# Kernel optimization log

Hardware: AMD Instinct MI355X
Metric: run time of the kernel (lower is better)

## Reference

```python
import jax, jax.numpy as jnp
import numpy as np

H = 10                 # heads in both convs
EPS = 1e-5             # GraphNorm eps
N, E, D_NODE, D_EDGE, G = 100000, 1600000, 128, 32, 64


def _lin(key, out_d, in_d, bias=True):
    k1, k2 = jax.random.split(key)
    W = jax.random.normal(k1, (out_d, in_d), jnp.float32) / np.sqrt(in_d)
    if bias:
        b = jax.random.normal(k2, (out_d,), jnp.float32) * 0.01
        return W, b
    return W


def setup_inputs() -> dict:
    key = jax.random.key(0)
    ks = jax.random.split(key, 20)
    x = jax.random.normal(ks[0], (N, D_NODE), jnp.float32)
    edge_attr = jax.random.normal(ks[1], (E, D_EDGE), jnp.float32)
    edge_index = jax.random.randint(ks[2], (2, E), 0, N)
    batch_idx = jnp.sort(jax.random.randint(ks[3], (N,), 0, G))
    # conv1: in=128, out=5, heads=10
    q1W, q1b = _lin(ks[4], H * 5, D_NODE)
    k1W, k1b = _lin(ks[5], H * 5, D_NODE)
    v1W, v1b = _lin(ks[6], H * 5, D_NODE)
    e1W = _lin(ks[7], H * 5, D_EDGE, bias=False)
    s1W, s1b = _lin(ks[8], 5, D_NODE)        # lin_skip
    b1W = _lin(ks[9], 1, 3 * 5, bias=False)  # lin_beta
    # GraphNorm(5)
    gnW = jnp.ones((5,), jnp.float32)
    gnb = jnp.zeros((5,), jnp.float32)
    gnms = jnp.ones((5,), jnp.float32)       # mean_scale
    # conv2: in=5, out=1, heads=10
    q2W, q2b = _lin(ks[10], H * 1, 5)
    k2W, k2b = _lin(ks[11], H * 1, 5)
    v2W, v2b = _lin(ks[12], H * 1, 5)
    e2W = _lin(ks[13], H * 1, D_EDGE, bias=False)
    s2W, s2b = _lin(ks[14], 1, 5)
    b2W = _lin(ks[15], 1, 3 * 1, bias=False)
    return dict(x=x, edge_attr=edge_attr, edge_index=edge_index, batch_idx=batch_idx,
                q1W=q1W, q1b=q1b, k1W=k1W, k1b=k1b, v1W=v1W, v1b=v1b, e1W=e1W,
                s1W=s1W, s1b=s1b, b1W=b1W, gnW=gnW, gnb=gnb, gnms=gnms,
                q2W=q2W, q2b=q2b, k2W=k2W, k2b=k2b, v2W=v2W, v2b=v2b, e2W=e2W,
                s2W=s2W, s2b=s2b, b2W=b2W)


def _tconv(x, src, dst, edge_attr, qW, qb, kW, kb, vW, vb, eW, sW, sb, bW, c):
    """PyG TransformerConv: concat=False, beta=True, eval (dropout off)."""
    n = x.shape[0]
    q = (x @ qW.T + qb).reshape(n, H, c)
    k = (x @ kW.T + kb).reshape(n, H, c)
    v = (x @ vW.T + vb).reshape(n, H, c)
    e = (edge_attr @ eW.T).reshape(-1, H, c)            # [E,H,c]
    kj = k[src] + e                                      # gather + edge bias
    alpha = jnp.einsum('ehc,ehc->eh', q[dst], kj) / np.sqrt(c)
    amax = jax.lax.stop_gradient(jax.ops.segment_max(alpha, dst, num_segments=n))
    ex = jnp.exp(alpha - amax[dst])
    denom = jax.ops.segment_sum(ex, dst, num_segments=n)
    a = ex / denom[dst]                                  # segment softmax [E,H]
    out = jax.ops.segment_sum((v[src] + e) * a[:, :, None], dst, num_segments=n)
    out = out.mean(axis=1)                               # concat=False -> head mean [N,c]
    xr = x @ sW.T + sb                                   # skip
    beta = jax.nn.sigmoid(jnp.concatenate([out, xr, out - xr], -1) @ bW.T)
    return beta * xr + (1.0 - beta) * out


def _graph_norm(x, batch, w, b, ms):
    cnt = jnp.maximum(jax.ops.segment_sum(jnp.ones((x.shape[0],), x.dtype), batch,
                                          num_segments=G), 1.0)[:, None]
    mean = jax.ops.segment_sum(x, batch, num_segments=G) / cnt
    out = x - mean[batch] * ms
    var = jax.ops.segment_sum(out * out, batch, num_segments=G) / cnt
    return w * out / jnp.sqrt(var + EPS)[batch] + b


def reference(x, edge_attr, edge_index, batch_idx,
              q1W, q1b, k1W, k1b, v1W, v1b, e1W, s1W, s1b, b1W,
              gnW, gnb, gnms,
              q2W, q2b, k2W, k2b, v2W, v2b, e2W, s2W, s2b, b2W):
    src, dst = edge_index[0], edge_index[1]
    h = _tconv(x, src, dst, edge_attr, q1W, q1b, k1W, k1b, v1W, v1b, e1W,
               s1W, s1b, b1W, 5)
    h = jax.nn.relu(_graph_norm(h, batch_idx, gnW, gnb, gnms))
    out = _tconv(h, src, dst, edge_attr, q2W, q2b, k2W, k2b, v2W, v2b, e2W,
                 s2W, s2b, b2W, 1)
    return jax.nn.sigmoid(out)
```

## Files before the change

### kernel.cpp

```cpp
#include <hip/hip_runtime.h>
#include <math.h>


#define EPS 1e-5f
#define INV_SQRT5 0.44721359549995794f

__device__ __forceinline__ float f16_to_f32(unsigned short u) {
  union { unsigned short us; _Float16 h; } cv; cv.us = u;
  return (float)cv.h;
}

__device__ __forceinline__ void store40(const float (&acc)[40], int n, int g,
                                        float* __restrict__ q1, float* __restrict__ kv1,
                                        float* __restrict__ xr1) {
#pragma unroll
  for (int c = 0; c < 40; ++c) {
    int ch = g * 40 + c;
    if (ch < 50)        q1[(size_t)n * 52 + ch] = acc[c];
    else if (ch < 100)  kv1[(size_t)n * 104 + 2 * (ch - 50)] = acc[c];
    else if (ch < 150)  kv1[(size_t)n * 104 + 2 * (ch - 100) + 1] = acc[c];
    else if (ch < 155)  xr1[(size_t)n * 8 + (ch - 150)] = acc[c];
  }
}

__global__ __launch_bounds__(256, 3) void k_qkvs1(
    const float* __restrict__ x,
    const float* __restrict__ qW, const float* __restrict__ qb,
    const float* __restrict__ kW, const float* __restrict__ kb,
    const float* __restrict__ vW, const float* __restrict__ vb,
    const float* __restrict__ sW, const float* __restrict__ sb,
    float* __restrict__ q1, float* __restrict__ kv1,
    float* __restrict__ xr1, int n_nodes) {
  __shared__ __align__(16) float sWt[40 * 128];
  __shared__ __align__(16) float sX[512 * 20];
  __shared__ float sB[40];
  const int t = threadIdx.x;
  const int g = blockIdx.y;
  const int n0 = blockIdx.x * 512;

  for (int i = t; i < 1280; i += 256) {
    int c = i >> 5, q = i & 31;
    int ch = g * 40 + c;
    float4 w = make_float4(0.f, 0.f, 0.f, 0.f);
    const float* srcr = nullptr;
    if (ch < 50)        srcr = qW + ch * 128;
    else if (ch < 100)  srcr = kW + (ch - 50) * 128;
    else if (ch < 150)  srcr = vW + (ch - 100) * 128;
    else if (ch < 155)  srcr = sW + (ch - 150) * 128;
    if (srcr) w = *(const float4*)(srcr + q * 4);
    *(float4*)&sWt[c * 128 + q * 4] = w;
  }
  if (t < 40) {
    int ch = g * 40 + t;
    float b = 0.f;
    if (ch < 50) b = qb[ch];
    else if (ch < 100) b = kb[ch - 50];
    else if (ch < 150) b = vb[ch - 100];
    else if (ch < 155) b = sb[ch - 150];
    sB[t] = b;
  }
  __syncthreads();

  float accA[40], accB[40];
#pragma unroll
  for (int c = 0; c < 40; ++c) { accA[c] = sB[c]; accB[c] = sB[c]; }
  const int na = n0 + 2 * t, nb = na + 1;
  const float4* w4 = (const float4*)sWt;

  for (int kc = 0; kc < 128; kc += 16) {
    __syncthreads();
#pragma unroll
    for (int i = 0; i < 8; ++i) {
      int idx = t + 256 * i;
      int r = idx >> 2, q = idx & 3;
      int n = n0 + r;
      float4 v = make_float4(0.f, 0.f, 0.f, 0.f);
      if (n < n_nodes) v = *(const float4*)(x + (size_t)n * 128 + kc + q * 4);
      *(float4*)&sX[r * 20 + q * 4] = v;
    }
    __syncthreads();
    float4 xa[4], xb[4];
#pragma unroll
    for (int q = 0; q < 4; ++q) {
      xa[q] = *(const float4*)&sX[(2 * t) * 20 + q * 4];
      xb[q] = *(const float4*)&sX[(2 * t + 1) * 20 + q * 4];
    }
    int base = kc >> 2;
#pragma unroll
    for (int c = 0; c < 40; ++c) {
#pragma unroll
      for (int q = 0; q < 4; ++q) {
        float4 w = w4[c * 32 + base + q];
        accA[c] = fmaf(w.x, xa[q].x, accA[c]); accA[c] = fmaf(w.y, xa[q].y, accA[c]);
        accA[c] = fmaf(w.z, xa[q].z, accA[c]); accA[c] = fmaf(w.w, xa[q].w, accA[c]);
        accB[c] = fmaf(w.x, xb[q].x, accB[c]); accB[c] = fmaf(w.y, xb[q].y, accB[c]);
        accB[c] = fmaf(w.z, xb[q].z, accB[c]); accB[c] = fmaf(w.w, xb[q].w, accB[c]);
      }
    }
  }
  if (na < n_nodes) store40(accA, na, g, q1, kv1, xr1);
  if (nb < n_nodes) store40(accB, nb, g, q1, kv1, xr1);
}

__global__ __launch_bounds__(256) void k_hist(const int* __restrict__ ei, int n_edges,
                                              int* __restrict__ cnt) {
  int e = blockIdx.x * 256 + threadIdx.x;
  if (e < n_edges) atomicAdd(&cnt[ei[n_edges + e]], 1);
}

__global__ __launch_bounds__(1024) void k_scan(const int* __restrict__ cnt,
                                               int* __restrict__ rp,
                                               int* __restrict__ cursor, int n) {
  __shared__ int ls[1024];
  int tid = threadIdx.x;
  const int CH = (((n + 1023) / 1024) + 3) & ~3;
  int lo = tid * CH, hi = min(lo + CH, n);
  int s = 0;
  if (lo < n) {
    int full = (hi - lo) & ~3;
    const int4* c4 = (const int4*)(cnt + lo);
    for (int i = 0; i < full; i += 4) {
      int4 v = c4[i >> 2];
      s += v.x + v.y + v.z + v.w;
    }
    for (int i = lo + full; i < hi; ++i) s += cnt[i];
  }
  ls[tid] = s;
  __syncthreads();
  for (int off = 1; off < 1024; off <<= 1) {
    int v = (tid >= off) ? ls[tid - off] : 0;
    __syncthreads();
    ls[tid] += v;
    __syncthreads();
  }
  int run = (tid > 0) ? ls[tid - 1] : 0;
  for (int i = lo; i < hi; ++i) {
    rp[i] = run; cursor[i] = run; run += cnt[i];
  }
  if (hi == n && lo < n) rp[n] = run;
}

__global__ __launch_bounds__(256) void k_scatter(const int* __restrict__ ei, int n_edges,
                                                 int* __restrict__ cursor,
                                                 int* __restrict__ seid,
                                                 int* __restrict__ ssrc) {
  int e = blockIdx.x * 256 + threadIdx.x;
  if (e >= n_edges) return;
  int s = ei[e];
  int d = ei[n_edges + e];
  int p = atomicAdd(&cursor[d], 1);
  seid[p] = e;
  ssrc[p] = s;
}

__global__ __launch_bounds__(256) void k_evt(
    float* attr, const float* __restrict__ e1W, const float* __restrict__ e2W,
    int n_edges) {
  int e = blockIdx.x * 256 + threadIdx.x;
  if (e >= n_edges) return;
  const float4* ar = (const float4*)(attr + (size_t)e * 32);
  float4 a[8];
#pragma unroll
  for (int j = 0; j < 8; ++j) a[j] = ar[j];
  unsigned int d[30];
#pragma unroll
  for (int c2 = 0; c2 < 30; ++c2) {
    int c0 = 2 * c2, c1 = 2 * c2 + 1;
    const float* w0 = (c0 < 50) ? (e1W + c0 * 32) : (e2W + (c0 - 50) * 32);
    const float* w1 = (c1 < 50) ? (e1W + c1 * 32) : (e2W + (c1 - 50) * 32);
    float acc0 = 0.f, acc1 = 0.f;
#pragma unroll
    for (int j = 0; j < 8; ++j) {
      float4 wa = *(const float4*)(w0 + 4 * j);
      float4 wb = *(const float4*)(w1 + 4 * j);
      acc0 = fmaf(wa.x, a[j].x, acc0); acc0 = fmaf(wa.y, a[j].y, acc0);
      acc0 = fmaf(wa.z, a[j].z, acc0); acc0 = fmaf(wa.w, a[j].w, acc0);
      acc1 = fmaf(wb.x, a[j].x, acc1); acc1 = fmaf(wb.y, a[j].y, acc1);
      acc1 = fmaf(wb.z, a[j].z, acc1); acc1 = fmaf(wb.w, a[j].w, acc1);
    }
    union { _Float16 h[2]; unsigned int u; } p;
    p.h[0] = (_Float16)acc0; p.h[1] = (_Float16)acc1;
    d[c2] = p.u;
  }
  unsigned int* row = (unsigned int*)(attr + (size_t)e * 32);
#pragma unroll
  for (int k = 0; k < 7; ++k)
    *(uint4*)(row + 4 * k) = make_uint4(d[4 * k], d[4 * k + 1], d[4 * k + 2], d[4 * k + 3]);
  *(uint2*)(row + 28) = make_uint2(d[28], d[29]);
}

__global__ __launch_bounds__(256) void k_conv1(
    const int* __restrict__ rp, const int* __restrict__ seid,
    const int* __restrict__ ssrc, const float* __restrict__ attr,
    const float* __restrict__ q1, const float* __restrict__ kv1,
    const float* __restrict__ xr1,
    const float* __restrict__ bW, float* __restrict__ h1, int n_nodes) {
  const int lane = threadIdx.x & 63;
  const int wid = (blockIdx.x * 256 + threadIdx.x) >> 6;
  const int nw = gridDim.x * 4;
  const int wr = (lane < 50) ? lane : 0;
  const int g0 = (wr / 5) * 5;
  const int cp = lane % 5;
  const unsigned short* evr = (const unsigned short*)attr;

  for (int n = wid; n < n_nodes; n += nw) {
    const int p0 = rp[n], deg = rp[n + 1] - p0;
    const float qc = q1[(size_t)n * 52 + wr];
    int eL = 0, sL = 0;
    if (lane < deg) { eL = seid[p0 + lane]; sL = ssrc[p0 + lane]; }
    float accN = 0.f, accD = 0.f;
    for (int i = 0; i < deg; ++i) {
      int e, s;
      if (i < 64) { e = __shfl(eL, i); s = __shfl(sL, i); }
      else        { e = seid[p0 + i]; s = ssrc[p0 + i]; }
      float ev = f16_to_f32(evr[(size_t)e * 64 + wr]);
      float2 kv = *(const float2*)(kv1 + (size_t)s * 104 + 2 * wr);
      float t = qc * (kv.x + ev);
      float al = __shfl(t, g0) + __shfl(t, g0 + 1) + __shfl(t, g0 + 2)
               + __shfl(t, g0 + 3) + __shfl(t, g0 + 4);
      float ex = __expf(al * INV_SQRT5);
      accD += ex;
      accN = fmaf(kv.y + ev, ex, accN);
    }
    float r = (accD > 0.f) ? accN / accD : 0.f;
    if (lane >= 50) r = 0.f;
    float o = 0.f;
#pragma unroll
    for (int h = 0; h < 10; ++h) o += __shfl(r, cp + 5 * h);
    o *= 0.1f;
    float xr = xr1[(size_t)n * 8 + cp];
    float tb = bW[cp] * o + bW[5 + cp] * xr + bW[10 + cp] * (o - xr);
    float sb = 0.f;
#pragma unroll
    for (int j = 0; j < 5; ++j) sb += __shfl(tb, j);
    float beta = 1.f / (1.f + __expf(-sb));
    if (lane < 5) h1[(size_t)n * 8 + lane] = beta * xr + (1.f - beta) * o;
  }
}

__global__ __launch_bounds__(256) void k_stats(
    const float* __restrict__ h1, const int* __restrict__ batch,
    float* __restrict__ gsum, float* __restrict__ gsq,
    float* __restrict__ gcnt, int n_nodes) {
  int n = blockIdx.x * 256 + threadIdx.x;
  bool act = n < n_nodes;
  int g = act ? batch[n] : 0;
  float v[5], s2[5], one = act ? 1.f : 0.f;
#pragma unroll
  for (int c = 0; c < 5; ++c) {
    v[c] = act ? h1[(size_t)n * 8 + c] : 0.f;
    s2[c] = v[c] * v[c];
  }
  int g0 = __shfl(g, 0);
  bool uni = __all((!act) || (g == g0));
  if (uni) {
#pragma unroll
    for (int off = 32; off; off >>= 1) {
#pragma unroll
      for (int c = 0; c < 5; ++c) {
        v[c] += __shfl_down(v[c], off);
        s2[c] += __shfl_down(s2[c], off);
      }
      one += __shfl_down(one, off);
    }
    if ((threadIdx.x & 63) == 0) {
#pragma unroll
      for (int c = 0; c < 5; ++c) {
        atomicAdd(&gsum[g0 * 8 + c], v[c]);
        atomicAdd(&gsq[g0 * 8 + c], s2[c]);
      }
      atomicAdd(&gcnt[g0], one);
    }
  } else if (act) {
#pragma unroll
    for (int c = 0; c < 5; ++c) {
      atomicAdd(&gsum[g * 8 + c], v[c]);
      atomicAdd(&gsq[g * 8 + c], s2[c]);
    }
    atomicAdd(&gcnt[g], 1.f);
  }
}

__global__ __launch_bounds__(256) void k_apply(
    const float* __restrict__ h1, const int* __restrict__ batch,
    const float* __restrict__ gsum, const float* __restrict__ gsq,
    const float* __restrict__ gcnt,
    const float* __restrict__ gnw, const float* __restrict__ gnb,
    const float* __restrict__ gnms,
    const float* __restrict__ q2W, const float* __restrict__ q2b,
    const float* __restrict__ k2W, const float* __restrict__ k2b,
    const float* __restrict__ v2W, const float* __restrict__ v2b,
    const float* __restrict__ s2W, const float* __restrict__ s2b,
    float* __restrict__ q2, float* __restrict__ kv2,
    float* __restrict__ xr2, int n_nodes) {
  int n = blockIdx.x * 256 + threadIdx.x;
  if (n >= n_nodes) return;
  int g = batch[n];
  float rc = 1.f / fmaxf(gcnt[g], 1.f);
  float r[5];
#pragma unroll
  for (int c = 0; c < 5; ++c) {
    float ms = gnms[c];
    float mean = gsum[g * 8 + c] * rc;
    float var = gsq[g * 8 + c] * rc - mean * mean * ms * (2.f - ms);
    var = fmaxf(var, 0.f);
    float o = h1[(size_t)n * 8 + c] - mean * ms;
    float y = gnw[c] * o * rsqrtf(var + EPS) + gnb[c];
    r[c] = fmaxf(y, 0.f);
  }
#pragma unroll
  for (int h = 0; h < 10; ++h) {
    float aq = q2b[h], ak = k2b[h], av = v2b[h];
#pragma unroll
    for (int i = 0; i < 5; ++i) {
      aq = fmaf(r[i], q2W[h * 5 + i], aq);
      ak = fmaf(r[i], k2W[h * 5 + i], ak);
      av = fmaf(r[i], v2W[h * 5 + i], av);
    }
    q2[(size_t)n * 12 + h] = aq;
    kv2[(size_t)n * 24 + 2 * h]     = ak;
    kv2[(size_t)n * 24 + 2 * h + 1] = av;
  }
  float s = s2b[0];
#pragma unroll
  for (int i = 0; i < 5; ++i) s = fmaf(r[i], s2W[i], s);
  xr2[n] = s;
}

__global__ __launch_bounds__(256) void k_conv2(
    const int* __restrict__ rp, const int* __restrict__ seid,
    const int* __restrict__ ssrc, const float* __restrict__ attr,
    const float* __restrict__ q2, const float* __restrict__ kv2,
    const float* __restrict__ xr2,
    const float* __restrict__ bW, float* __restrict__ out, int n_nodes) {
  const int lane = threadIdx.x & 63;
  const int wid = (blockIdx.x * 256 + threadIdx.x) >> 6;
  const int nw = gridDim.x * 4;
  const int slot = lane / 10, h = lane - slot * 10;
  const bool active = slot < 6;
  const unsigned short* evr = (const unsigned short*)attr;

  for (int n = wid; n < n_nodes; n += nw) {
    int p0 = rp[n], deg = rp[n + 1] - p0;
    float qh = q2[(size_t)n * 12 + h];
    int eL = 0, sL = 0;
    if (lane < deg) { eL = seid[p0 + lane]; sL = ssrc[p0 + lane]; }
    float accN = 0.f, accD = 0.f;
    int nit = (deg + 5) / 6;
    for (int t = 0; t < nit; ++t) {
      int i = t * 6 + slot;
      bool val = active && (i < deg);
      int e = 0, s = 0;
      if (i < 64) { e = __shfl(eL, i); s = __shfl(sL, i); }
      else if (val) { e = seid[p0 + i]; s = ssrc[p0 + i]; }
      float evv = 0.f; float2 kv = make_float2(0.f, 0.f);
      if (val) {
        evv = f16_to_f32(evr[(size_t)e * 64 + 50 + h]);
        kv = *(const float2*)(kv2 + (size_t)s * 24 + 2 * h);
      }
      float exv = val ? __expf(qh * (kv.x + evv)) : 0.f;
      accD += exv;
      accN = fmaf(kv.y + evv, exv, accN);
    }
    float D = 0.f, Nn = 0.f;
#pragma unroll
    for (int i2 = 0; i2 < 6; ++i2) {
      D  += __shfl(accD, h + 10 * i2);
      Nn += __shfl(accN, h + 10 * i2);
    }
    float r = (D > 0.f) ? Nn / D : 0.f;
    float o = 0.f;
#pragma unroll
    for (int j = 0; j < 10; ++j) o += __shfl(r, j);
    o *= 0.1f;
    float xr = xr2[n];
    float sbv = bW[0] * o + bW[1] * xr + bW[2] * (o - xr);
    float beta = 1.f / (1.f + __expf(-sbv));
    float y = beta * xr + (1.f - beta) * o;
    if (lane == 0) out[n] = 1.f / (1.f + __expf(-y));
  }
}

extern "C" void kernel_launch(void* const* d_in, const int* in_sizes, int n_in,
                              void* d_out, int out_size, void* d_ws, size_t ws_size,
                              hipStream_t stream) {
  const float* x    = (const float*)d_in[0];
  float*       attr = (float*)d_in[1];
  const int*   ei   = (const int*)d_in[2];
  const int*   batch= (const int*)d_in[3];
  const float* q1W = (const float*)d_in[4];  const float* q1b = (const float*)d_in[5];
  const float* k1W = (const float*)d_in[6];  const float* k1b = (const float*)d_in[7];
  const float* v1W = (const float*)d_in[8];  const float* v1b = (const float*)d_in[9];
  const float* e1W = (const float*)d_in[10];
  const float* s1W = (const float*)d_in[11]; const float* s1b = (const float*)d_in[12];
  const float* b1W = (const float*)d_in[13];
  const float* gnW = (const float*)d_in[14]; const float* gnb = (const float*)d_in[15];
  const float* gnms= (const float*)d_in[16];
  const float* q2W = (const float*)d_in[17]; const float* q2b = (const float*)d_in[18];
  const float* k2W = (const float*)d_in[19]; const float* k2b = (const float*)d_in[20];
  const float* v2W = (const float*)d_in[21]; const float* v2b = (const float*)d_in[22];
  const float* e2W = (const float*)d_in[23];
  const float* s2W = (const float*)d_in[24]; const float* s2b = (const float*)d_in[25];
  const float* b2W = (const float*)d_in[26];

  const int n_nodes = in_sizes[0] / 128;
  const int n_edges = in_sizes[2] / 2;
  float* ws = (float*)d_ws;
  const size_t nn = (size_t)n_nodes;
  const size_t ne = (size_t)n_edges;

  const size_t oQ1  = 0;
  const size_t oKV1 = 52 * nn;
  const size_t oXR1 = 156 * nn;
  const size_t oH1  = 164 * nn;
  const size_t oQ2  = 172 * nn;
  const size_t oKV2 = 184 * nn;
  const size_t oXR2 = 208 * nn;
  const size_t oSTAT= 209 * nn;
  const size_t oCNT = oSTAT + 1088;
  const size_t oRP  = oCNT + nn;
  const size_t oCUR = oRP + nn + 1;
  const size_t oSEID= oCUR + nn;
  const size_t oSSRC= oSEID + ne;

  int* cnt    = (int*)(ws + oCNT);
  int* rp     = (int*)(ws + oRP);
  int* cursor = (int*)(ws + oCUR);
  int* seid   = (int*)(ws + oSEID);
  int* ssrc   = (int*)(ws + oSSRC);
  float* gsum = ws + oSTAT;
  float* gsq  = ws + oSTAT + 512;
  float* gcnt = ws + oSTAT + 1024;

  const int nb_nodes = (n_nodes + 255) / 256;
  const int nb_edges = (n_edges + 255) / 256;
  dim3 gq((n_nodes + 511) / 512, 4);
  const int nb_pers = 2048;

  hipMemsetAsync(ws + oSTAT, 0, (1088 + nn) * sizeof(float), stream);

  k_hist<<<nb_edges, 256, 0, stream>>>(ei, n_edges, cnt);
  k_scan<<<1, 1024, 0, stream>>>(cnt, rp, cursor, n_nodes);
  k_scatter<<<nb_edges, 256, 0, stream>>>(ei, n_edges, cursor, seid, ssrc);

  k_qkvs1<<<gq, 256, 0, stream>>>(x, q1W, q1b, k1W, k1b, v1W, v1b, s1W, s1b,
                                  ws + oQ1, ws + oKV1, ws + oXR1, n_nodes);
  k_evt<<<nb_edges, 256, 0, stream>>>(attr, e1W, e2W, n_edges);

  k_conv1<<<nb_pers, 256, 0, stream>>>(rp, seid, ssrc, attr,
                                       ws + oQ1, ws + oKV1, ws + oXR1,
                                       b1W, ws + oH1, n_nodes);
  k_stats<<<nb_nodes, 256, 0, stream>>>(ws + oH1, batch, gsum, gsq, gcnt, n_nodes);
  k_apply<<<nb_nodes, 256, 0, stream>>>(ws + oH1, batch, gsum, gsq, gcnt,
                                        gnW, gnb, gnms,
                                        q2W, q2b, k2W, k2b, v2W, v2b, s2W, s2b,
                                        ws + oQ2, ws + oKV2, ws + oXR2, n_nodes);
  k_conv2<<<nb_pers, 256, 0, stream>>>(rp, seid, ssrc, attr,
                                       ws + oQ2, ws + oKV2, ws + oXR2,
                                       b2W, (float*)d_out, n_nodes);
}
```

Baseline: 1.302 ms.

## Load x directly into registers in QKV GEMM and unroll edge loop by two

New measurement: 1.248 ms. 1.04x faster.

```diff
diff --git a/kernel.cpp b/kernel.cpp
--- a/kernel.cpp
+++ b/kernel.cpp
@@ -23,7 +23,7 @@
   }
 }
 
-__global__ __launch_bounds__(256, 3) void k_qkvs1(
+__global__ __launch_bounds__(256, 4) void k_qkvs1(
     const float* __restrict__ x,
     const float* __restrict__ qW, const float* __restrict__ qb,
     const float* __restrict__ kW, const float* __restrict__ kb,
@@ -32,7 +32,6 @@
     float* __restrict__ q1, float* __restrict__ kv1,
     float* __restrict__ xr1, int n_nodes) {
   __shared__ __align__(16) float sWt[40 * 128];
-  __shared__ __align__(16) float sX[512 * 20];
   __shared__ float sB[40];
   const int t = threadIdx.x;
   const int g = blockIdx.y;
@@ -65,41 +64,33 @@
 #pragma unroll
   for (int c = 0; c < 40; ++c) { accA[c] = sB[c]; accB[c] = sB[c]; }
   const int na = n0 + 2 * t, nb = na + 1;
+  const bool okA = na < n_nodes, okB = nb < n_nodes;
+  const float* xa_p = x + (size_t)(okA ? na : 0) * 128;
+  const float* xb_p = x + (size_t)(okB ? nb : 0) * 128;
   const float4* w4 = (const float4*)sWt;
 
-  for (int kc = 0; kc < 128; kc += 16) {
-    __syncthreads();
-#pragma unroll
-    for (int i = 0; i < 8; ++i) {
-      int idx = t + 256 * i;
-      int r = idx >> 2, q = idx & 3;
-      int n = n0 + r;
-      float4 v = make_float4(0.f, 0.f, 0.f, 0.f);
-      if (n < n_nodes) v = *(const float4*)(x + (size_t)n * 128 + kc + q * 4);
-      *(float4*)&sX[r * 20 + q * 4] = v;
-    }
-    __syncthreads();
-    float4 xa[4], xb[4];
-#pragma unroll
-    for (int q = 0; q < 4; ++q) {
-      xa[q] = *(const float4*)&sX[(2 * t) * 20 + q * 4];
-      xb[q] = *(const float4*)&sX[(2 * t + 1) * 20 + q * 4];
-    }
-    int base = kc >> 2;
+  for (int kc = 0; kc < 128; kc += 8) {
+    float4 xa0 = *(const float4*)(xa_p + kc);
+    float4 xa1 = *(const float4*)(xa_p + kc + 4);
+    float4 xb0 = *(const float4*)(xb_p + kc);
+    float4 xb1 = *(const float4*)(xb_p + kc + 4);
+    const int base = kc >> 2;
 #pragma unroll
     for (int c = 0; c < 40; ++c) {
-#pragma unroll
-      for (int q = 0; q < 4; ++q) {
-        float4 w = w4[c * 32 + base + q];
-        accA[c] = fmaf(w.x, xa[q].x, accA[c]); accA[c] = fmaf(w.y, xa[q].y, accA[c]);
-        accA[c] = fmaf(w.z, xa[q].z, accA[c]); accA[c] = fmaf(w.w, xa[q].w, accA[c]);
-        accB[c] = fmaf(w.x, xb[q].x, accB[c]); accB[c] = fmaf(w.y, xb[q].y, accB[c]);
-        accB[c] = fmaf(w.z, xb[q].z, accB[c]); accB[c] = fmaf(w.w, xb[q].w, accB[c]);
-      }
-    }
-  }
-  if (na < n_nodes) store40(accA, na, g, q1, kv1, xr1);
-  if (nb < n_nodes) store40(accB, nb, g, q1, kv1, xr1);
+      float4 w0 = w4[c * 32 + base];
+      float4 w1 = w4[c * 32 + base + 1];
+      accA[c] = fmaf(w0.x, xa0.x, accA[c]); accA[c] = fmaf(w0.y, xa0.y, accA[c]);
+      accA[c] = fmaf(w0.z, xa0.z, accA[c]); accA[c] = fmaf(w0.w, xa0.w, accA[c]);
+      accA[c] = fmaf(w1.x, xa1.x, accA[c]); accA[c] = fmaf(w1.y, xa1.y, accA[c]);
+      accA[c] = fmaf(w1.z, xa1.z, accA[c]); accA[c] = fmaf(w1.w, xa1.w, accA[c]);
+      accB[c] = fmaf(w0.x, xb0.x, accB[c]); accB[c] = fmaf(w0.y, xb0.y, accB[c]);
+      accB[c] = fmaf(w0.z, xb0.z, accB[c]); accB[c] = fmaf(w0.w, xb0.w, accB[c]);
+      accB[c] = fmaf(w1.x, xb1.x, accB[c]); accB[c] = fmaf(w1.y, xb1.y, accB[c]);
+      accB[c] = fmaf(w1.z, xb1.z, accB[c]); accB[c] = fmaf(w1.w, xb1.w, accB[c]);
+    }
+  }
+  if (okA) store40(accA, na, g, q1, kv1, xr1);
+  if (okB) store40(accB, nb, g, q1, kv1, xr1);
 }
 
 __global__ __launch_bounds__(256) void k_hist(const int* __restrict__ ei, int n_edges,
@@ -208,20 +199,45 @@
     const float qc = q1[(size_t)n * 52 + wr];
     int eL = 0, sL = 0;
     if (lane < deg) { eL = seid[p0 + lane]; sL = ssrc[p0 + lane]; }
-    float accN = 0.f, accD = 0.f;
-    for (int i = 0; i < deg; ++i) {
-      int e, s;
-      if (i < 64) { e = __shfl(eL, i); s = __shfl(sL, i); }
-      else        { e = seid[p0 + i]; s = ssrc[p0 + i]; }
+    float accN0 = 0.f, accD0 = 0.f, accN1 = 0.f, accD1 = 0.f;
+    int i = 0;
+    for (; i + 2 <= deg; i += 2) {
+      int e0, s0, e1, s1;
+      if (i + 1 < 64) {
+        e0 = __shfl(eL, i);     s0 = __shfl(sL, i);
+        e1 = __shfl(eL, i + 1); s1 = __shfl(sL, i + 1);
+      } else {
+        e0 = (i < 64) ? __shfl(eL, i) : seid[p0 + i];
+        s0 = (i < 64) ? __shfl(sL, i) : ssrc[p0 + i];
+        e1 = seid[p0 + i + 1];  s1 = ssrc[p0 + i + 1];
+      }
+      float ev0 = f16_to_f32(evr[(size_t)e0 * 64 + wr]);
+      float ev1 = f16_to_f32(evr[(size_t)e1 * 64 + wr]);
+      float2 kva = *(const float2*)(kv1 + (size_t)s0 * 104 + 2 * wr);
+      float2 kvb = *(const float2*)(kv1 + (size_t)s1 * 104 + 2 * wr);
+      float t0 = qc * (kva.x + ev0);
+      float t1 = qc * (kvb.x + ev1);
+      float al0 = __shfl(t0, g0) + __shfl(t0, g0 + 1) + __shfl(t0, g0 + 2)
+                + __shfl(t0, g0 + 3) + __shfl(t0, g0 + 4);
+      float al1 = __shfl(t1, g0) + __shfl(t1, g0 + 1) + __shfl(t1, g0 + 2)
+                + __shfl(t1, g0 + 3) + __shfl(t1, g0 + 4);
+      float ex0 = __expf(al0 * INV_SQRT5);
+      float ex1 = __expf(al1 * INV_SQRT5);
+      accD0 += ex0; accN0 = fmaf(kva.y + ev0, ex0, accN0);
+      accD1 += ex1; accN1 = fmaf(kvb.y + ev1, ex1, accN1);
+    }
+    if (i < deg) {
+      int e = (i < 64) ? __shfl(eL, i) : seid[p0 + i];
+      int s = (i < 64) ? __shfl(sL, i) : ssrc[p0 + i];
       float ev = f16_to_f32(evr[(size_t)e * 64 + wr]);
       float2 kv = *(const float2*)(kv1 + (size_t)s * 104 + 2 * wr);
       float t = qc * (kv.x + ev);
       float al = __shfl(t, g0) + __shfl(t, g0 + 1) + __shfl(t, g0 + 2)
                + __shfl(t, g0 + 3) + __shfl(t, g0 + 4);
       float ex = __expf(al * INV_SQRT5);
-      accD += ex;
-      accN = fmaf(kv.y + ev, ex, accN);
-    }
+      accD0 += ex; accN0 = fmaf(kv.y + ev, ex, accN0);
+    }
+    float accN = accN0 + accN1, accD = accD0 + accD1;
     float r = (accD > 0.f) ? accN / accD : 0.f;
     if (lane >= 50) r = 0.f;
     float o = 0.f;
```
